# Performance work log

Measured on AMD Instinct MI355X. Metric: run time of the kernel, lower is better.

The kernel has to match this reference:

```python
import jax, jax.numpy as jnp
import numpy as np
from jax import lax

SEQ_LEN, N_FEAT, N_EMB, N_ENC, BATCH = 100, 18, 16, 16, 16384


def lstm(x, W_ih, W_hh, b_ih, b_hh, hidden):
    """PyTorch-convention LSTM (gates i,f,g,o), batch_first x: [B,T,I].
    Returns (h_seq [B,T,H], h_last [B,H])."""
    B = x.shape[0]
    # Precompute input projections for all timesteps: [B,T,4H]
    xg = jnp.einsum('bti,gi->btg', x, W_ih) + b_ih + b_hh
    W_hh_T = W_hh.T  # [H,4H]

    def step(carry, xg_t):
        h, c = carry
        g = xg_t + h @ W_hh_T                       # [B,4H]
        i, f, gg, o = jnp.split(g, 4, axis=-1)
        i = jax.nn.sigmoid(i)
        f = jax.nn.sigmoid(f)
        gg = jnp.tanh(gg)
        o = jax.nn.sigmoid(o)
        c = f * c + i * gg
        h = o * jnp.tanh(c)
        return (h, c), h

    h0 = jnp.zeros((B, hidden), x.dtype)
    c0 = jnp.zeros((B, hidden), x.dtype)
    (h_last, _), h_seq = lax.scan(step, (h0, c0), jnp.swapaxes(xg, 0, 1))
    return jnp.swapaxes(h_seq, 0, 1), h_last


def setup_inputs() -> dict:
    key = jax.random.key(0)
    ks = jax.random.split(key, 9)
    s1 = 1.0 / np.sqrt(N_EMB)
    s2 = 1.0 / np.sqrt(N_ENC)
    u = lambda k, shape, s: jax.random.uniform(k, shape, jnp.float32, -s, s)
    return {
        'x': jax.random.normal(ks[0], (BATCH, SEQ_LEN, N_FEAT), jnp.float32),
        'W_ih1': u(ks[1], (4 * N_EMB, N_FEAT), s1),
        'W_hh1': u(ks[2], (4 * N_EMB, N_EMB), s1),
        'b_ih1': u(ks[3], (4 * N_EMB,), s1),
        'b_hh1': u(ks[4], (4 * N_EMB,), s1),
        'W_ih2': u(ks[5], (4 * N_ENC, N_EMB), s2),
        'W_hh2': u(ks[6], (4 * N_ENC, N_ENC), s2),
        'b_ih2': u(ks[7], (4 * N_ENC,), s2),
        'b_hh2': u(ks[8], (4 * N_ENC,), s2),
    }


def reference(x, W_ih1, W_hh1, b_ih1, b_hh1, W_ih2, W_hh2, b_ih2, b_hh2):
    h1_seq, _ = lstm(x, W_ih1, W_hh1, b_ih1, b_hh1, N_EMB)
    h1_seq = jax.nn.relu(h1_seq)
    _, h2_last = lstm(h1_seq, W_ih2, W_hh2, b_ih2, b_hh2, N_ENC)
    return jax.nn.relu(h2_last)  # [B, N_ENC]
```

## Files before the change

### kernel.cpp

```cpp
#include <hip/hip_runtime.h>


typedef float f32x4 __attribute__((ext_vector_type(4)));
typedef __bf16 bf16x8 __attribute__((ext_vector_type(8)));
typedef unsigned int uint32x4 __attribute__((ext_vector_type(4)));

union FragU { bf16x8 v; unsigned short u[8]; unsigned int d[4]; uint32x4 q; };

#define MFMA16(A, B, C) __builtin_amdgcn_mfma_f32_16x16x32_bf16((A), (B), (C), 0, 0, 0)

static __device__ __forceinline__ unsigned short f2bf(float f) {
  unsigned int u = __builtin_bit_cast(unsigned int, f);
  u = u + 0x7FFFu + ((u >> 16) & 1u);
  return (unsigned short)(u >> 16);
}
static __device__ __forceinline__ float bfbits2f(unsigned short h) {
  unsigned int u = ((unsigned int)h) << 16;
  return __builtin_bit_cast(float, u);
}
static __device__ __forceinline__ float sigm(float x) {
  return __builtin_amdgcn_rcpf(1.0f + __builtin_amdgcn_exp2f(x * -1.4426950408889634f));
}
static __device__ __forceinline__ float tanh_(float x) {
  return 1.0f - 2.0f * __builtin_amdgcn_rcpf(1.0f + __builtin_amdgcn_exp2f(x * 2.8853900817779268f));
}
static __device__ __forceinline__ unsigned int split_pack(float v) {
  unsigned int u = __builtin_bit_cast(unsigned int, v);
  float hf = __builtin_bit_cast(float, u & 0xFFFF0000u);
  unsigned int l = __builtin_bit_cast(unsigned int, v - hf);
  return (u >> 16) | (l & 0xFFFF0000u);
}
static __device__ __forceinline__ void cvt_pair(float f0, float f1,
                                                unsigned int& hd, unsigned int& ld) {
  unsigned int u0 = __builtin_bit_cast(unsigned int, f0);
  unsigned int u1 = __builtin_bit_cast(unsigned int, f1);
  unsigned int h0 = u0 & 0xFFFF0000u;
  unsigned int h1 = u1 & 0xFFFF0000u;
  hd = (u0 >> 16) | h1;
  unsigned int l0 = __builtin_bit_cast(unsigned int, f0 - __builtin_bit_cast(float, h0));
  unsigned int l1 = __builtin_bit_cast(unsigned int, f1 - __builtin_bit_cast(float, h1));
  ld = (l0 >> 16) | (l1 & 0xFFFF0000u);
}

struct RawX { float2 a, b2, c, d; };

__global__ __launch_bounds__(256, 1) void enc_kernel(
    const float* __restrict__ x,
    const float* __restrict__ Wih1,
    const float* __restrict__ Whh1,
    const float* __restrict__ bih1,
    const float* __restrict__ bhh1,
    const float* __restrict__ Wih2,
    const float* __restrict__ Whh2,
    const float* __restrict__ bih2,
    const float* __restrict__ bhh2,
    float* __restrict__ out)
{
  const int lane = threadIdx.x & 63;
  const int b    = lane & 15;
  const int g    = lane >> 4;

  const int wid = (int)((blockIdx.x * blockDim.x + threadIdx.x) >> 6);
  const int b0  = wid * 16;

  FragU A1h[4], A1l[4], A2h[4], A2l[4], A3h[4], A3l[4], A4h[4], A4l[4];
  f32x4 bias1v[4], bias2v[4];
#pragma unroll
  for (int tn = 0; tn < 4; ++tn) {
    const int row = tn * 16 + b;
#pragma unroll
    for (int j = 0; j < 8; ++j) {
      const int k = 8 * g + j;
      if (k < 18) {
        const float w = Wih1[row * 18 + k];
        A1h[tn].u[j] = f2bf(w);
        A1l[tn].u[j] = f2bf(w - bfbits2f(A1h[tn].u[j]));
      } else {
        A1h[tn].u[j] = 0;
        A1l[tn].u[j] = 0;
      }
      const int kk = k >> 1;
      const float w2 = Whh1[row * 16 + kk];
      const float w3 = Wih2[row * 16 + kk];
      const float w4 = Whh2[row * 16 + kk];
      A2h[tn].u[j] = f2bf(w2); A2l[tn].u[j] = f2bf(w2 - bfbits2f(A2h[tn].u[j]));
      A3h[tn].u[j] = f2bf(w3); A3l[tn].u[j] = f2bf(w3 - bfbits2f(A3h[tn].u[j]));
      A4h[tn].u[j] = f2bf(w4); A4l[tn].u[j] = f2bf(w4 - bfbits2f(A4h[tn].u[j]));
    }
#pragma unroll
    for (int r = 0; r < 4; ++r) {
      const int u4 = tn * 16 + 4 * g + r;
      bias1v[tn][r] = bih1[u4] + bhh1[u4];
      bias2v[tn][r] = bih2[u4] + bhh2[u4];
    }
  }

  const float* const x0 = x + (size_t)(b0 + b) * 1800 + 8 * g;
  const int adv = (g == 3) ? 0 : 18;

  auto loadraw = [&](const float* p) -> RawX {
    RawX r;
    r.a = *(const float2*)p;
    if (g < 2) {
      r.b2 = *(const float2*)(p + 2);
      r.c  = *(const float2*)(p + 4);
      r.d  = *(const float2*)(p + 6);
    } else {
      r.b2 = r.c = r.d = make_float2(0.f, 0.f);
    }
    return r;
  };
  auto cvt = [&](const RawX& rw, FragU& hi, FragU& lo) {
    cvt_pair(rw.a.x, rw.a.y, hi.d[0], lo.d[0]);
    cvt_pair(rw.b2.x, rw.b2.y, hi.d[1], lo.d[1]);
    cvt_pair(rw.c.x, rw.c.y, hi.d[2], lo.d[2]);
    cvt_pair(rw.d.x, rw.d.y, hi.d[3], lo.d[3]);
  };

  RawX rw0 = loadraw(x0);
  RawX rw1 = loadraw(x0 + adv);
  RawX rw  = loadraw(x0 + 2 * adv);
  const float* xq = x0 + 3 * adv;

  FragU hb, h2b;
  hb.q  = (uint32x4){0u, 0u, 0u, 0u};
  h2b.q = (uint32x4){0u, 0u, 0u, 0u};
  float c1[4] = {0.f, 0.f, 0.f, 0.f};
  float c2[4] = {0.f, 0.f, 0.f, 0.f};
  float h2v[4] = {0.f, 0.f, 0.f, 0.f};

  FragU xch, xcl;
  cvt(rw0, xch, xcl);

  f32x4 ga[4];
#pragma unroll
  for (int tn = 0; tn < 4; ++tn) {
    f32x4 acc = MFMA16(A1h[tn].v, xch.v, bias1v[tn]);
    acc = MFMA16(A1l[tn].v, xch.v, acc);
    acc = MFMA16(A1h[tn].v, xcl.v, acc);
    acc = MFMA16(A2h[tn].v, hb.v, acc);
    acc = MFMA16(A2l[tn].v, hb.v, acc);
    ga[tn] = acc;
  }
  cvt(rw1, xch, xcl);

#pragma unroll 2
  for (int t = 0; t < 100; ++t) {
    FragU rb;
#pragma unroll
    for (int r = 0; r < 4; ++r) {
      const float iv = sigm(ga[0][r]);
      const float fv = sigm(ga[1][r]);
      const float gv = tanh_(ga[2][r]);
      const float ov = sigm(ga[3][r]);
      const float cc = fv * c1[r] + iv * gv;
      c1[r] = cc;
      const float h = ov * tanh_(cc);
      const unsigned int pk = split_pack(h);
      hb.d[r] = pk;
      rb.d[r] = (h > 0.f) ? pk : 0u;
    }

    f32x4 gb[4];
#pragma unroll
    for (int tn = 0; tn < 4; ++tn) {
      f32x4 acc = MFMA16(A4h[tn].v, h2b.v, bias2v[tn]);
      acc = MFMA16(A4l[tn].v, h2b.v, acc);
      acc = MFMA16(A3h[tn].v, rb.v, acc);
      acc = MFMA16(A3l[tn].v, rb.v, acc);
      gb[tn] = acc;
    }

    f32x4 gan[4];
#pragma unroll
    for (int tn = 0; tn < 4; ++tn) {
      f32x4 acc = MFMA16(A1h[tn].v, xch.v, bias1v[tn]);
      acc = MFMA16(A1l[tn].v, xch.v, acc);
      acc = MFMA16(A1h[tn].v, xcl.v, acc);
      acc = MFMA16(A2h[tn].v, hb.v, acc);
      acc = MFMA16(A2l[tn].v, hb.v, acc);
      gan[tn] = acc;
    }

    FragU nxh, nxl;
    cvt(rw, nxh, nxl);

    RawX rwn = loadraw((t <= 96) ? xq : x0);
    xq += adv;

#pragma unroll
    for (int r = 0; r < 4; ++r) {
      const float iv = sigm(gb[0][r]);
      const float fv = sigm(gb[1][r]);
      const float gv = tanh_(gb[2][r]);
      const float ov = sigm(gb[3][r]);
      const float cc = fv * c2[r] + iv * gv;
      c2[r] = cc;
      const float h = ov * tanh_(cc);
      h2v[r] = h;
      h2b.d[r] = split_pack(h);
    }

#pragma unroll
    for (int tn = 0; tn < 4; ++tn) ga[tn] = gan[tn];
    xch = nxh;
    xcl = nxl;
    rw = rwn;
  }

  f32x4 o;
#pragma unroll
  for (int r = 0; r < 4; ++r) o[r] = fmaxf(h2v[r], 0.f);
  *(f32x4*)(out + (size_t)(b0 + b) * 16 + 4 * g) = o;

  (void)x0;
}

extern "C" void kernel_launch(void* const* d_in, const int* in_sizes, int n_in,
                              void* d_out, int out_size, void* d_ws, size_t ws_size,
                              hipStream_t stream) {
  (void)in_sizes; (void)n_in; (void)d_ws; (void)ws_size; (void)out_size;
  enc_kernel<<<dim3(256), dim3(256), 0, stream>>>(
      (const float*)d_in[0],
      (const float*)d_in[1],
      (const float*)d_in[2],
      (const float*)d_in[3],
      (const float*)d_in[4],
      (const float*)d_in[5],
      (const float*)d_in[6],
      (const float*)d_in[7],
      (const float*)d_in[8],
      (float*)d_out);
}
```

Baseline: 268.3 us.

## Split LSTM layers across producer/consumer waves with LDS double-buffer handoff

Each block now holds 2 batch tiles. Waves 0-1 run layer 1 and write relu(h1) to a double-buffered LDS slot each step. Waves 2-3 read that slot and run layer 2, synchronised with __syncthreads. This pipelines the two layers on separate wavefronts and halves the weight registers each wave needs, allowing 2 blocks per CU and twice the grid. The cost is a block-wide barrier every timestep that couples all four waves, plus twice as many wavefronts in total.

Result: slower. 289.6 us (+8.0%).

```diff
diff --git a/kernel.cpp b/kernel.cpp
--- a/kernel.cpp
+++ b/kernel.cpp
@@ -44,7 +44,7 @@
 
 struct RawX { float2 a, b2, c, d; };
 
-__global__ __launch_bounds__(256, 1) void enc_kernel(
+__global__ __launch_bounds__(256, 2) void enc_kernel(
     const float* __restrict__ x,
     const float* __restrict__ Wih1,
     const float* __restrict__ Whh1,
@@ -56,122 +56,77 @@
     const float* __restrict__ bhh2,
     float* __restrict__ out)
 {
+  __shared__ __align__(16) uint32x4 buf[2][2][64];
+
+  const int wv   = threadIdx.x >> 6;
   const int lane = threadIdx.x & 63;
+  const int tile = wv & 1;
   const int b    = lane & 15;
   const int g    = lane >> 4;
-
-  const int wid = (int)((blockIdx.x * blockDim.x + threadIdx.x) >> 6);
-  const int b0  = wid * 16;
-
-  FragU A1h[4], A1l[4], A2h[4], A2l[4], A3h[4], A3l[4], A4h[4], A4l[4];
-  f32x4 bias1v[4], bias2v[4];
-#pragma unroll
-  for (int tn = 0; tn < 4; ++tn) {
-    const int row = tn * 16 + b;
-#pragma unroll
-    for (int j = 0; j < 8; ++j) {
-      const int k = 8 * g + j;
-      if (k < 18) {
-        const float w = Wih1[row * 18 + k];
-        A1h[tn].u[j] = f2bf(w);
-        A1l[tn].u[j] = f2bf(w - bfbits2f(A1h[tn].u[j]));
+  const int b0   = ((int)blockIdx.x * 2 + tile) * 16;
+
+  if (wv < 2) {
+    FragU A1h[4], A1l[4], A2h[4], A2l[4];
+    f32x4 bias1v[4];
+#pragma unroll
+    for (int tn = 0; tn < 4; ++tn) {
+      const int row = tn * 16 + b;
+#pragma unroll
+      for (int j = 0; j < 8; ++j) {
+        const int k = 8 * g + j;
+        if (k < 18) {
+          const float w = Wih1[row * 18 + k];
+          A1h[tn].u[j] = f2bf(w);
+          A1l[tn].u[j] = f2bf(w - bfbits2f(A1h[tn].u[j]));
+        } else {
+          A1h[tn].u[j] = 0;
+          A1l[tn].u[j] = 0;
+        }
+        const float w2 = Whh1[row * 16 + (k >> 1)];
+        A2h[tn].u[j] = f2bf(w2);
+        A2l[tn].u[j] = f2bf(w2 - bfbits2f(A2h[tn].u[j]));
+      }
+#pragma unroll
+      for (int r = 0; r < 4; ++r) {
+        const int u4 = tn * 16 + 4 * g + r;
+        bias1v[tn][r] = bih1[u4] + bhh1[u4];
+      }
+    }
+
+    const float* const x0 = x + (size_t)(b0 + b) * 1800 + 8 * g;
+    const int adv = (g == 3) ? 0 : 18;
+
+    auto loadraw = [&](const float* p) -> RawX {
+      RawX r;
+      r.a = *(const float2*)p;
+      if (g < 2) {
+        r.b2 = *(const float2*)(p + 2);
+        r.c  = *(const float2*)(p + 4);
+        r.d  = *(const float2*)(p + 6);
       } else {
-        A1h[tn].u[j] = 0;
-        A1l[tn].u[j] = 0;
-      }
-      const int kk = k >> 1;
-      const float w2 = Whh1[row * 16 + kk];
-      const float w3 = Wih2[row * 16 + kk];
-      const float w4 = Whh2[row * 16 + kk];
-      A2h[tn].u[j] = f2bf(w2); A2l[tn].u[j] = f2bf(w2 - bfbits2f(A2h[tn].u[j]));
-      A3h[tn].u[j] = f2bf(w3); A3l[tn].u[j] = f2bf(w3 - bfbits2f(A3h[tn].u[j]));
-      A4h[tn].u[j] = f2bf(w4); A4l[tn].u[j] = f2bf(w4 - bfbits2f(A4h[tn].u[j]));
-    }
-#pragma unroll
-    for (int r = 0; r < 4; ++r) {
-      const int u4 = tn * 16 + 4 * g + r;
-      bias1v[tn][r] = bih1[u4] + bhh1[u4];
-      bias2v[tn][r] = bih2[u4] + bhh2[u4];
-    }
-  }
-
-  const float* const x0 = x + (size_t)(b0 + b) * 1800 + 8 * g;
-  const int adv = (g == 3) ? 0 : 18;
-
-  auto loadraw = [&](const float* p) -> RawX {
-    RawX r;
-    r.a = *(const float2*)p;
-    if (g < 2) {
-      r.b2 = *(const float2*)(p + 2);
-      r.c  = *(const float2*)(p + 4);
-      r.d  = *(const float2*)(p + 6);
-    } else {
-      r.b2 = r.c = r.d = make_float2(0.f, 0.f);
-    }
-    return r;
-  };
-  auto cvt = [&](const RawX& rw, FragU& hi, FragU& lo) {
-    cvt_pair(rw.a.x, rw.a.y, hi.d[0], lo.d[0]);
-    cvt_pair(rw.b2.x, rw.b2.y, hi.d[1], lo.d[1]);
-    cvt_pair(rw.c.x, rw.c.y, hi.d[2], lo.d[2]);
-    cvt_pair(rw.d.x, rw.d.y, hi.d[3], lo.d[3]);
-  };
-
-  RawX rw0 = loadraw(x0);
-  RawX rw1 = loadraw(x0 + adv);
-  RawX rw  = loadraw(x0 + 2 * adv);
-  const float* xq = x0 + 3 * adv;
-
-  FragU hb, h2b;
-  hb.q  = (uint32x4){0u, 0u, 0u, 0u};
-  h2b.q = (uint32x4){0u, 0u, 0u, 0u};
-  float c1[4] = {0.f, 0.f, 0.f, 0.f};
-  float c2[4] = {0.f, 0.f, 0.f, 0.f};
-  float h2v[4] = {0.f, 0.f, 0.f, 0.f};
-
-  FragU xch, xcl;
-  cvt(rw0, xch, xcl);
-
-  f32x4 ga[4];
-#pragma unroll
-  for (int tn = 0; tn < 4; ++tn) {
-    f32x4 acc = MFMA16(A1h[tn].v, xch.v, bias1v[tn]);
-    acc = MFMA16(A1l[tn].v, xch.v, acc);
-    acc = MFMA16(A1h[tn].v, xcl.v, acc);
-    acc = MFMA16(A2h[tn].v, hb.v, acc);
-    acc = MFMA16(A2l[tn].v, hb.v, acc);
-    ga[tn] = acc;
-  }
-  cvt(rw1, xch, xcl);
-
-#pragma unroll 2
-  for (int t = 0; t < 100; ++t) {
-    FragU rb;
-#pragma unroll
-    for (int r = 0; r < 4; ++r) {
-      const float iv = sigm(ga[0][r]);
-      const float fv = sigm(ga[1][r]);
-      const float gv = tanh_(ga[2][r]);
-      const float ov = sigm(ga[3][r]);
-      const float cc = fv * c1[r] + iv * gv;
-      c1[r] = cc;
-      const float h = ov * tanh_(cc);
-      const unsigned int pk = split_pack(h);
-      hb.d[r] = pk;
-      rb.d[r] = (h > 0.f) ? pk : 0u;
-    }
-
-    f32x4 gb[4];
-#pragma unroll
-    for (int tn = 0; tn < 4; ++tn) {
-      f32x4 acc = MFMA16(A4h[tn].v, h2b.v, bias2v[tn]);
-      acc = MFMA16(A4l[tn].v, h2b.v, acc);
-      acc = MFMA16(A3h[tn].v, rb.v, acc);
-      acc = MFMA16(A3l[tn].v, rb.v, acc);
-      gb[tn] = acc;
-    }
-
-    f32x4 gan[4];
+        r.b2 = r.c = r.d = make_float2(0.f, 0.f);
+      }
+      return r;
+    };
+    auto cvt = [&](const RawX& rw_, FragU& hi, FragU& lo) {
+      cvt_pair(rw_.a.x,  rw_.a.y,  hi.d[0], lo.d[0]);
+      cvt_pair(rw_.b2.x, rw_.b2.y, hi.d[1], lo.d[1]);
+      cvt_pair(rw_.c.x,  rw_.c.y,  hi.d[2], lo.d[2]);
+      cvt_pair(rw_.d.x,  rw_.d.y,  hi.d[3], lo.d[3]);
+    };
+
+    RawX rw0 = loadraw(x0);
+    RawX rw1 = loadraw(x0 + adv);
+    RawX rw  = loadraw(x0 + 2 * adv);
+    const float* xq = x0 + 3 * adv;
+
+    FragU hb;  hb.q = (uint32x4){0u, 0u, 0u, 0u};
+    float c1[4] = {0.f, 0.f, 0.f, 0.f};
+
+    FragU xch, xcl;
+    cvt(rw0, xch, xcl);
+
+    f32x4 ga[4];
 #pragma unroll
     for (int tn = 0; tn < 4; ++tn) {
       f32x4 acc = MFMA16(A1h[tn].v, xch.v, bias1v[tn]);
@@ -179,48 +134,107 @@
       acc = MFMA16(A1h[tn].v, xcl.v, acc);
       acc = MFMA16(A2h[tn].v, hb.v, acc);
       acc = MFMA16(A2l[tn].v, hb.v, acc);
-      gan[tn] = acc;
-    }
-
-    FragU nxh, nxl;
-    cvt(rw, nxh, nxl);
-
-    RawX rwn = loadraw((t <= 96) ? xq : x0);
-    xq += adv;
-
-#pragma unroll
-    for (int r = 0; r < 4; ++r) {
-      const float iv = sigm(gb[0][r]);
-      const float fv = sigm(gb[1][r]);
-      const float gv = tanh_(gb[2][r]);
-      const float ov = sigm(gb[3][r]);
-      const float cc = fv * c2[r] + iv * gv;
-      c2[r] = cc;
-      const float h = ov * tanh_(cc);
-      h2v[r] = h;
-      h2b.d[r] = split_pack(h);
-    }
-
-#pragma unroll
-    for (int tn = 0; tn < 4; ++tn) ga[tn] = gan[tn];
-    xch = nxh;
-    xcl = nxl;
-    rw = rwn;
+      ga[tn] = acc;
+    }
+    cvt(rw1, xch, xcl);
+
+#pragma unroll 2
+    for (int t = 0; t < 100; ++t) {
+      FragU rb;
+#pragma unroll
+      for (int r = 0; r < 4; ++r) {
+        const float iv = sigm(ga[0][r]);
+        const float fv = sigm(ga[1][r]);
+        const float gv = tanh_(ga[2][r]);
+        const float ov = sigm(ga[3][r]);
+        const float cc = fv * c1[r] + iv * gv;
+        c1[r] = cc;
+        const float h = ov * tanh_(cc);
+        const unsigned int pk = split_pack(h);
+        hb.d[r] = pk;
+        rb.d[r] = (h > 0.f) ? pk : 0u;
+      }
+      buf[tile][t & 1][lane] = rb.q;
+      __syncthreads();
+
+#pragma unroll
+      for (int tn = 0; tn < 4; ++tn) {
+        f32x4 acc = MFMA16(A1h[tn].v, xch.v, bias1v[tn]);
+        acc = MFMA16(A1l[tn].v, xch.v, acc);
+        acc = MFMA16(A1h[tn].v, xcl.v, acc);
+        acc = MFMA16(A2h[tn].v, hb.v, acc);
+        acc = MFMA16(A2l[tn].v, hb.v, acc);
+        ga[tn] = acc;
+      }
+      cvt(rw, xch, xcl);
+      rw = loadraw((t <= 96) ? xq : x0);
+      xq += adv;
+    }
+  } else {
+    FragU A3h[4], A3l[4], A4h[4], A4l[4];
+    f32x4 bias2v[4];
+#pragma unroll
+    for (int tn = 0; tn < 4; ++tn) {
+      const int row = tn * 16 + b;
+#pragma unroll
+      for (int j = 0; j < 8; ++j) {
+        const int kk = (8 * g + j) >> 1;
+        const float w3 = Wih2[row * 16 + kk];
+        const float w4 = Whh2[row * 16 + kk];
+        A3h[tn].u[j] = f2bf(w3); A3l[tn].u[j] = f2bf(w3 - bfbits2f(A3h[tn].u[j]));
+        A4h[tn].u[j] = f2bf(w4); A4l[tn].u[j] = f2bf(w4 - bfbits2f(A4h[tn].u[j]));
+      }
+#pragma unroll
+      for (int r = 0; r < 4; ++r) {
+        const int u4 = tn * 16 + 4 * g + r;
+        bias2v[tn][r] = bih2[u4] + bhh2[u4];
+      }
+    }
+
+    FragU h2b;  h2b.q = (uint32x4){0u, 0u, 0u, 0u};
+    float c2[4] = {0.f, 0.f, 0.f, 0.f};
+    float h2v[4] = {0.f, 0.f, 0.f, 0.f};
+
+#pragma unroll 2
+    for (int t = 0; t < 100; ++t) {
+      __syncthreads();
+      FragU rq;  rq.q = buf[tile][t & 1][lane];
+
+      f32x4 gb[4];
+#pragma unroll
+      for (int tn = 0; tn < 4; ++tn) {
+        f32x4 acc = MFMA16(A4h[tn].v, h2b.v, bias2v[tn]);
+        acc = MFMA16(A4l[tn].v, h2b.v, acc);
+        acc = MFMA16(A3h[tn].v, rq.v, acc);
+        acc = MFMA16(A3l[tn].v, rq.v, acc);
+        gb[tn] = acc;
+      }
+#pragma unroll
+      for (int r = 0; r < 4; ++r) {
+        const float iv = sigm(gb[0][r]);
+        const float fv = sigm(gb[1][r]);
+        const float gv = tanh_(gb[2][r]);
+        const float ov = sigm(gb[3][r]);
+        const float cc = fv * c2[r] + iv * gv;
+        c2[r] = cc;
+        const float h = ov * tanh_(cc);
+        h2v[r] = h;
+        h2b.d[r] = split_pack(h);
+      }
+    }
+
+    f32x4 o;
+#pragma unroll
+    for (int r = 0; r < 4; ++r) o[r] = fmaxf(h2v[r], 0.f);
+    *(f32x4*)(out + (size_t)(b0 + b) * 16 + 4 * g) = o;
   }
-
-  f32x4 o;
-#pragma unroll
-  for (int r = 0; r < 4; ++r) o[r] = fmaxf(h2v[r], 0.f);
-  *(f32x4*)(out + (size_t)(b0 + b) * 16 + 4 * g) = o;
-
-  (void)x0;
 }
 
 extern "C" void kernel_launch(void* const* d_in, const int* in_sizes, int n_in,
                               void* d_out, int out_size, void* d_ws, size_t ws_size,
                               hipStream_t stream) {
   (void)in_sizes; (void)n_in; (void)d_ws; (void)ws_size; (void)out_size;
-  enc_kernel<<<dim3(256), dim3(256), 0, stream>>>(
+  enc_kernel<<<dim3(512), dim3(256), 0, stream>>>(
       (const float*)d_in[0],
       (const float*)d_in[1],
       (const float*)d_in[2],
```
